# Kernel optimization log

Measured on AMD Instinct MI355X. Metric: run time of the kernel, lower is better.

The kernel has to match this reference:

```python
import jax, jax.numpy as jnp
import numpy as np

C_IN, C_OUT, H = 8, 8, 16
N1D = 20                      # 1D quadrature points -> 400 mesh nodes in 2D
B = 16
DECAY = (N1D / 4.0) ** 4      # set_quad: decay_param = (N/4)**4


def _quad_mesh():
    # Gauss-Legendre nodes/weights on [-1,1], tensor-product in 2D (get_quad_mesh)
    x, w = np.polynomial.legendre.leggauss(N1D)
    X, Y = np.meshgrid(x, x, indexing='xy')
    WX, WY = np.meshgrid(w, w, indexing='xy')
    nodes = np.dstack([X, Y]).reshape(-1, 2).astype(np.float32)
    weights = (WX * WY).reshape(-1).astype(np.float32)
    return nodes, weights


def setup_inputs() -> dict:
    key = jax.random.key(0)
    k1, k2, k3, k4 = jax.random.split(key, 4)
    nodes, w = _quad_mesh()
    K = C_IN * C_OUT
    return {
        'features': jax.random.normal(k1, (B, C_IN, N1D * N1D), jnp.float32),
        # 64 tiny MLPs (Linear no bias + Sin), spec (2,16,16,1), stacked on axis 0
        'W1': jax.random.normal(k2, (K, H, 2), jnp.float32) / np.sqrt(2.0),
        'W2': jax.random.normal(k3, (K, H, H), jnp.float32) / np.sqrt(float(H)),
        'W3': jax.random.normal(k4, (K, 1, H), jnp.float32) / np.sqrt(float(H)),
        'output_locs': jnp.asarray(nodes),   # (M,2) same tensor-product mesh
        'mesh_nodes': jnp.asarray(nodes),    # (N,2)
        'mesh_weights': jnp.asarray(w),      # (N,) product of 1D weights
    }


def _kernel(W1, W2, W3, output_locs, mesh_nodes):
    # pairwise eval points z = y_m - x_n, shape (M, N, 2)
    z = output_locs[:, None, :] - mesh_nodes[None, :, :]
    M, N, _ = z.shape
    zf = z.reshape(M * N, 2)
    # batched tiny MLPs: Linear -> Sin -> Linear -> Sin -> Linear (no bias)
    h = jnp.sin(jnp.einsum('khd,pd->kph', W1, zf))
    h = jnp.sin(jnp.einsum('koh,kph->kpo', W2, h))
    kv = jnp.einsum('koh,kph->kpo', W3, h)[..., 0]          # (K, M*N)
    # bump function enforcing compact support: exp(1 - 1/(1 - c*||z||^4))
    bump_arg = jnp.sum(zf * zf, axis=-1) ** 2               # ||z||^4
    inside = bump_arg < 1.0 / DECAY
    safe = jnp.where(inside, 1.0 - DECAY * bump_arg, 1.0)
    bump = jnp.where(inside, jnp.exp(1.0 - 1.0 / safe), 0.0)
    kv = kv * bump[None, :]
    return kv.reshape(C_OUT, C_IN, M, N)


def reference(features, W1, W2, W3, output_locs, mesh_nodes, mesh_weights):
    Kmat = _kernel(W1, W2, W3, output_locs, mesh_nodes)     # (Co,Ci,M,N)
    # quadrature-weighted conv sum: out[b,o,m] = sum_{i,n} K[o,i,m,n] w[n] f[b,i,n]
    return jnp.einsum('oimn,n,bin->bom', Kmat, mesh_weights, features)
```

## Files before the change

### kernel.cpp

```cpp
#include <hip/hip_runtime.h>
#include <math.h>

#define CIN   8
#define COUT  8
#define HH    16
#define NN    400
#define MM    400
#define BB    16

#define THREADS 512
#define GM      2
#define PMAX    32

#define WS_FT 0
#define WS_ZX (NN*CIN*BB)
#define WS_ZY (WS_ZX + MM*PMAX)
#define WS_BW (WS_ZY + MM*PMAX)
#define WS_PN (WS_BW + MM*PMAX)

__global__ __launch_bounds__(THREADS) void prep_kernel(
    const float* __restrict__ f,
    const float* __restrict__ locs,
    const float* __restrict__ nodes,
    const float* __restrict__ wq,
    float* __restrict__ ws)
{
    const int blk = blockIdx.x;
    const int t   = threadIdx.x;

    if (blk < 100) {
        int idx = blk * 512 + t;
        int n = idx >> 7, c = idx & 127;
        int i = c >> 4, b = c & 15;
        ws[WS_FT + idx] = f[b * (CIN*NN) + i * NN + n];
    } else {
        const int lane = t & 63;
        const int w    = t >> 6;
        const int m    = (blk - 100) * 8 + w;
        const float2 y = ((const float2*)locs)[m];
        const float2* nd = (const float2*)nodes;
        int cnt = 0;
        for (int n0 = 0; n0 < NN; n0 += 64) {
            int n = n0 + lane;
            bool in = false;
            float zx = 0.f, zy = 0.f, bwv = 0.f;
            if (n < NN) {
                float2 x = nd[n];
                zx = y.x - x.x; zy = y.y - x.y;
                float s = zx*zx + zy*zy;
                float a = s * s;
                if (a < (1.0f/625.0f)) {
                    in = true;
                    bwv = __expf(1.0f - 1.0f/(1.0f - 625.0f*a)) * wq[n];
                }
            }
            unsigned long long msk = __ballot(in);
            int idx = cnt + __popcll(msk & ((1ull << lane) - 1ull));
            if (in && idx < PMAX) {
                ws[WS_ZX + m*PMAX + idx] = zx;
                ws[WS_ZY + m*PMAX + idx] = zy;
                ws[WS_BW + m*PMAX + idx] = bwv;
                ((int*)ws)[WS_PN + m*PMAX + idx] = n;
            }
            cnt += __popcll(msk);
        }
        if (lane >= cnt && lane < PMAX) {
            ws[WS_ZX + m*PMAX + lane] = 0.f;
            ws[WS_ZY + m*PMAX + lane] = 0.f;
            ws[WS_BW + m*PMAX + lane] = 0.f;
            ((int*)ws)[WS_PN + m*PMAX + lane] = 0;
        }
    }
}

__global__ __launch_bounds__(THREADS, 8) void quadconv_kernel(
    const float* __restrict__ W1,
    const float* __restrict__ W2,
    const float* __restrict__ W3,
    const float* __restrict__ ws,
    float* __restrict__ out)
{
    __shared__ float s_kv[8*64];
    __shared__ float s_part[8*32];
    __shared__ int   s_pn[GM*PMAX];

    const int t    = threadIdx.x;
    const int lane = t & 63;
    const int w    = __builtin_amdgcn_readfirstlane(t >> 6);
    const int pg   = blockIdx.x >> 3;
    const int kg   = blockIdx.x & 7;
    const int m0   = pg * GM;

    const float zx = ws[WS_ZX + m0*PMAX + lane];
    const float zy = ws[WS_ZY + m0*PMAX + lane];
    const float bw = ws[WS_BW + m0*PMAX + lane];
    if (t < GM*PMAX) s_pn[t] = ((const int*)ws)[WS_PN + m0*PMAX + t];

    {
        const int k = kg * 8 + w;
        const float* __restrict__ w1 = W1 + k * (HH * 2);
        const float* __restrict__ w2 = W2 + k * (HH * HH);
        const float* __restrict__ w3 = W3 + k * HH;

        float h1[HH];
        #pragma unroll
        for (int j = 0; j < HH; ++j)
            h1[j] = __sinf(w1[2*j] * zx + w1[2*j + 1] * zy);

        float kv = 0.f;
        #pragma unroll
        for (int oo = 0; oo < HH; ++oo) {
            float d = 0.f;
            #pragma unroll
            for (int j = 0; j < HH; ++j)
                d += w2[oo*HH + j] * h1[j];
            kv += w3[oo] * __sinf(d);
        }
        s_kv[w*64 + lane] = kv * bw;
    }
    __syncthreads();

    {
        const int b    = lane & 15;
        const int g    = (lane >> 4) & 1;
        const int half = lane >> 5;
        const float* __restrict__ ftp = ws + WS_FT;
        float acc = 0.f;
        #pragma unroll
        for (int jj = 0; jj < PMAX/2; ++jj) {
            int   sl = g*PMAX + half*(PMAX/2) + jj;
            int   n  = s_pn[sl];
            float kv = s_kv[w*64 + sl];
            acc += kv * ftp[n*128 + w*16 + b];
        }
        acc += __shfl_xor(acc, 32);
        if (half == 0)
            s_part[w*32 + lane] = acc;
    }
    __syncthreads();

    if (t < 32) {
        const int b = t & 15, g = t >> 4;
        float v = 0.f;
        #pragma unroll
        for (int ww = 0; ww < 8; ++ww)
            v += s_part[ww*32 + t];
        out[b * (COUT*MM) + kg * MM + (m0 + g)] = v;
    }
}

extern "C" void kernel_launch(void* const* d_in, const int* in_sizes, int n_in,
                              void* d_out, int out_size, void* d_ws, size_t ws_size,
                              hipStream_t stream) {
    const float* f     = (const float*)d_in[0];
    const float* W1    = (const float*)d_in[1];
    const float* W2    = (const float*)d_in[2];
    const float* W3    = (const float*)d_in[3];
    const float* locs  = (const float*)d_in[4];
    const float* nodes = (const float*)d_in[5];
    const float* wq    = (const float*)d_in[6];
    float* out = (float*)d_out;
    float* ws  = (float*)d_ws;

    prep_kernel<<<dim3(150), dim3(THREADS), 0, stream>>>(f, locs, nodes, wq, ws);
    quadconv_kernel<<<dim3((MM/GM) * COUT), dim3(THREADS), 0, stream>>>(
        W1, W2, W3, ws, out);
}
```

Baseline: 23.55 us.

## Persistent quadconv blocks with prefetched packed neighbor lists and coalesced transpose

```diff
diff --git a/kernel.cpp b/kernel.cpp
--- a/kernel.cpp
+++ b/kernel.cpp
@@ -11,12 +11,10 @@
 #define THREADS 512
 #define GM      2
 #define PMAX    32
+#define NPG     (MM/GM)
 
 #define WS_FT 0
-#define WS_ZX (NN*CIN*BB)
-#define WS_ZY (WS_ZX + MM*PMAX)
-#define WS_BW (WS_ZY + MM*PMAX)
-#define WS_PN (WS_BW + MM*PMAX)
+#define WS_L  (NN*CIN*BB)
 
 __global__ __launch_bounds__(THREADS) void prep_kernel(
     const float* __restrict__ f,
@@ -30,15 +28,18 @@
 
     if (blk < 100) {
         int idx = blk * 512 + t;
-        int n = idx >> 7, c = idx & 127;
-        int i = c >> 4, b = c & 15;
-        ws[WS_FT + idx] = f[b * (CIN*NN) + i * NN + n];
+        int b = idx / 3200;
+        int r = idx - b * 3200;
+        int i = r / 400;
+        int n = r - i * 400;
+        ws[WS_FT + n*128 + i*16 + b] = f[idx];
     } else {
         const int lane = t & 63;
         const int w    = t >> 6;
         const int m    = (blk - 100) * 8 + w;
         const float2 y = ((const float2*)locs)[m];
         const float2* nd = (const float2*)nodes;
+        float4* lst = (float4*)(ws + WS_L);
         int cnt = 0;
         for (int n0 = 0; n0 < NN; n0 += 64) {
             int n = n0 + lane;
@@ -56,20 +57,12 @@
             }
             unsigned long long msk = __ballot(in);
             int idx = cnt + __popcll(msk & ((1ull << lane) - 1ull));
-            if (in && idx < PMAX) {
-                ws[WS_ZX + m*PMAX + idx] = zx;
-                ws[WS_ZY + m*PMAX + idx] = zy;
-                ws[WS_BW + m*PMAX + idx] = bwv;
-                ((int*)ws)[WS_PN + m*PMAX + idx] = n;
-            }
+            if (in && idx < PMAX)
+                lst[m*PMAX + idx] = make_float4(zx, zy, bwv, __int_as_float(n));
             cnt += __popcll(msk);
         }
-        if (lane >= cnt && lane < PMAX) {
-            ws[WS_ZX + m*PMAX + lane] = 0.f;
-            ws[WS_ZY + m*PMAX + lane] = 0.f;
-            ws[WS_BW + m*PMAX + lane] = 0.f;
-            ((int*)ws)[WS_PN + m*PMAX + lane] = 0;
-        }
+        if (lane >= cnt && lane < PMAX)
+            lst[m*PMAX + lane] = make_float4(0.f, 0.f, 0.f, __int_as_float(0));
     }
 }
 
@@ -82,70 +75,82 @@
 {
     __shared__ float s_kv[8*64];
     __shared__ float s_part[8*32];
-    __shared__ int   s_pn[GM*PMAX];
+    __shared__ int   s_pn[2][64];
 
     const int t    = threadIdx.x;
     const int lane = t & 63;
     const int w    = __builtin_amdgcn_readfirstlane(t >> 6);
-    const int pg   = blockIdx.x >> 3;
-    const int kg   = blockIdx.x & 7;
-    const int m0   = pg * GM;
+    const int kg   = blockIdx.x >> 6;
+    const int pb   = blockIdx.x & 63;
 
-    const float zx = ws[WS_ZX + m0*PMAX + lane];
-    const float zy = ws[WS_ZY + m0*PMAX + lane];
-    const float bw = ws[WS_BW + m0*PMAX + lane];
-    if (t < GM*PMAX) s_pn[t] = ((const int*)ws)[WS_PN + m0*PMAX + t];
+    const int k = kg * 8 + w;
+    const float* __restrict__ w1 = W1 + k * (HH * 2);
+    const float* __restrict__ w2 = W2 + k * (HH * HH);
+    const float* __restrict__ w3 = W3 + k * HH;
 
-    {
-        const int k = kg * 8 + w;
-        const float* __restrict__ w1 = W1 + k * (HH * 2);
-        const float* __restrict__ w2 = W2 + k * (HH * HH);
-        const float* __restrict__ w3 = W3 + k * HH;
+    const int b    = lane & 15;
+    const int g    = (lane >> 4) & 1;
+    const int half = lane >> 5;
+    const float* __restrict__ ftp = ws + WS_FT;
+    const float4* __restrict__ lst = (const float4*)(ws + WS_L);
 
-        float h1[HH];
-        #pragma unroll
-        for (int j = 0; j < HH; ++j)
-            h1[j] = __sinf(w1[2*j] * zx + w1[2*j + 1] * zy);
+    int pg = pb;
+    float4 sv = lst[pg*64 + lane];
+    if (t < 64) s_pn[0][t] = __float_as_int(sv.w);
+    __syncthreads();
 
-        float kv = 0.f;
-        #pragma unroll
-        for (int oo = 0; oo < HH; ++oo) {
-            float d = 0.f;
+    int par = 0;
+    for (; pg < NPG; pg += 64, par ^= 1) {
+        {
+            const float zx = sv.x, zy = sv.y, bw = sv.z;
+            float h1[HH];
             #pragma unroll
             for (int j = 0; j < HH; ++j)
-                d += w2[oo*HH + j] * h1[j];
-            kv += w3[oo] * __sinf(d);
+                h1[j] = __sinf(w1[2*j] * zx + w1[2*j + 1] * zy);
+
+            float kv = 0.f;
+            #pragma unroll
+            for (int oo = 0; oo < HH; ++oo) {
+                float d = 0.f;
+                #pragma unroll
+                for (int j = 0; j < HH; ++j)
+                    d += w2[oo*HH + j] * h1[j];
+                kv += w3[oo] * __sinf(d);
+            }
+            s_kv[w*64 + lane] = kv * bw;
         }
-        s_kv[w*64 + lane] = kv * bw;
-    }
-    __syncthreads();
 
-    {
-        const int b    = lane & 15;
-        const int g    = (lane >> 4) & 1;
-        const int half = lane >> 5;
-        const float* __restrict__ ftp = ws + WS_FT;
-        float acc = 0.f;
-        #pragma unroll
-        for (int jj = 0; jj < PMAX/2; ++jj) {
-            int   sl = g*PMAX + half*(PMAX/2) + jj;
-            int   n  = s_pn[sl];
-            float kv = s_kv[w*64 + sl];
-            acc += kv * ftp[n*128 + w*16 + b];
+        const int pgN = pg + 64;
+        float4 svN = make_float4(0.f, 0.f, 0.f, 0.f);
+        if (pgN < NPG) svN = lst[pgN*64 + lane];
+
+        __syncthreads();
+
+        {
+            float acc = 0.f;
+            #pragma unroll
+            for (int jj = 0; jj < PMAX/2; ++jj) {
+                int   sl = g*PMAX + half*(PMAX/2) + jj;
+                int   n  = s_pn[par][sl];
+                acc += s_kv[w*64 + sl] * ftp[n*128 + w*16 + b];
+            }
+            acc += __shfl_xor(acc, 32);
+            if (half == 0)
+                s_part[w*32 + lane] = acc;
         }
-        acc += __shfl_xor(acc, 32);
-        if (half == 0)
-            s_part[w*32 + lane] = acc;
-    }
-    __syncthreads();
+        if (pgN < NPG && t < 64) s_pn[par ^ 1][t] = __float_as_int(svN.w);
 
-    if (t < 32) {
-        const int b = t & 15, g = t >> 4;
-        float v = 0.f;
-        #pragma unroll
-        for (int ww = 0; ww < 8; ++ww)
-            v += s_part[ww*32 + t];
-        out[b * (COUT*MM) + kg * MM + (m0 + g)] = v;
+        __syncthreads();
+
+        if (t < 32) {
+            const int bb = t & 15, gg = t >> 4;
+            float v = 0.f;
+            #pragma unroll
+            for (int ww = 0; ww < 8; ++ww)
+                v += s_part[ww*32 + t];
+            out[bb * (COUT*MM) + kg * MM + (pg*GM + gg)] = v;
+        }
+        sv = svN;
     }
 }
 
@@ -163,6 +168,5 @@
     float* ws  = (float*)d_ws;
 
     prep_kernel<<<dim3(150), dim3(THREADS), 0, stream>>>(f, locs, nodes, wq, ws);
-    quadconv_kernel<<<dim3((MM/GM) * COUT), dim3(THREADS), 0, stream>>>(
-        W1, W2, W3, ws, out);
+    quadconv_kernel<<<dim3(512), dim3(THREADS), 0, stream>>>(W1, W2, W3, ws, out);
 }
```

Result: slower. 38.06 us (+61.6%).
